# Optimization experiments

Hardware: AMD Instinct MI355X
Metric: run time of the kernel (lower is better)

The kernel has to match this reference:

```python
import jax, jax.numpy as jnp
import numpy as np

SINKHORN_ITERS = 50  # fixed iteration count (original uses err-tolerance while-loop)


def sinkhorn(M, a, b, lam):
    # M: [T, V] cost; a: [T, B] topic marginals; b: [V, B] word marginals
    K = jnp.exp(-M * lam)            # [T, V]
    u0 = jnp.ones_like(a) / a.shape[0]

    def step(u, _):
        v = b / (K.T @ u)            # [V, B]
        u = a / (K @ v)              # [T, B]
        return u, None

    u, _ = jax.lax.scan(step, u0, None, length=SINKHORN_ITERS)
    v = b / (K.T @ u)
    # per-document sinkhorn divergence: sum_t u_t * ((K*M) @ v)_t -> [B]
    return jnp.sum(u * ((K * M) @ v), axis=0)


def setup_inputs() -> dict:
    key = jax.random.key(0)
    kx, kt, kw, km, ke = jax.random.split(key, 5)
    B, T, V, E = 2048, 100, 20000, 256
    x = jax.random.uniform(kx, (B, V), dtype=jnp.float32)  # BoW-like weights
    doc_topic = jax.random.uniform(kt, (B, T), dtype=jnp.float32) + 1e-3
    doc_topic = doc_topic / jnp.sum(doc_topic, axis=1, keepdims=True)
    doc_word = jax.random.uniform(kw, (B, V), dtype=jnp.float32) + 1e-3
    doc_word = doc_word / jnp.sum(doc_word, axis=1, keepdims=True)
    M = jax.random.uniform(km, (T, V), dtype=jnp.float32)  # nonneg cost in [0,1)
    topic_embedding = jax.random.normal(ke, (T, E), dtype=jnp.float32)
    return {"x": x, "doc_topic": doc_topic, "doc_word": doc_word, "M": M,
            "topic_embedding": topic_embedding, "sh_alpha": 20,
            "rec_loss_weight": 100}


def reference(x, doc_topic, doc_word, M, topic_embedding, sh_alpha, rec_loss_weight):
    sh_loss = sinkhorn(M, doc_topic.T, doc_word.T, sh_alpha).mean()
    rec_log_probs = jax.nn.log_softmax(doc_topic @ (1.0 - M), axis=1)  # [B, V]
    rec_loss = -jnp.mean(jnp.sum(rec_log_probs * x, axis=1))
    joint_loss = rec_loss_weight * rec_loss + sh_loss
    return (rec_loss, sh_loss, joint_loss)
```

## Files before the change

### kernel.cpp

```cpp
#include <hip/hip_runtime.h>
#include <math.h>

#define B_   2048
#define T_   100
#define V_   20000
#define VP   20480
#define KP   128
#define TP   112
#define NC2  32
#define CH2  640
#define LDV  72
#define RXB  16

typedef short s8v __attribute__((ext_vector_type(8)));
typedef short s4v __attribute__((ext_vector_type(4)));
typedef float f4  __attribute__((ext_vector_type(4)));

__device__ __forceinline__ short f2bf(float f) {
    unsigned u = __builtin_bit_cast(unsigned, f);
    u += 0x7fffu + ((u >> 16) & 1u);
    return (short)(u >> 16);
}
__device__ __forceinline__ float bf2f(short h) {
    unsigned u = ((unsigned)(unsigned short)h) << 16;
    return __builtin_bit_cast(float, u);
}
#define MFMA(a,b,c) __builtin_amdgcn_mfma_f32_16x16x32_bf16((a),(b),(c),0,0,0)

__global__ void k_initKT(const float* __restrict__ M, const int* __restrict__ alpha,
                         short* __restrict__ A1, short* __restrict__ W1) {
    __shared__ float tile[32][33];
    float lam = (float)(*alpha);
    int v0 = blockIdx.x * 32, t0 = blockIdx.y * 32;
    int tx = threadIdx.x, ty = threadIdx.y;
    for (int j = 0; j < 4; ++j) {
        int t = t0 + ty + 8 * j, v = v0 + tx;
        tile[ty + 8 * j][tx] = (t < T_ && v < V_) ? M[(size_t)t * V_ + v] : 0.f;
    }
    __syncthreads();
    for (int j = 0; j < 4; ++j) {
        int t = t0 + tx, v = v0 + ty + 8 * j;
        float m = tile[tx][ty + 8 * j];
        bool valid = (t < T_) && (v < V_);
        A1[(size_t)v * KP + t] = valid ? f2bf(__expf(-m * lam)) : (short)0;
        W1[(size_t)v * KP + t] = valid ? f2bf(1.f - m) : (short)0;
    }
}

__global__ void k_initA2(const float* __restrict__ M, const int* __restrict__ alpha,
                         short* __restrict__ A2, short* __restrict__ A2M) {
    float lam = (float)(*alpha);
    size_t id = (size_t)blockIdx.x * 256 + threadIdx.x;
    int t = (int)(id / VP), v = (int)(id % VP);
    bool valid = (t < T_) && (v < V_);
    float m = valid ? M[(size_t)t * V_ + v] : 0.f;
    float k = valid ? __expf(-m * lam) : 0.f;
    A2[id]  = valid ? f2bf(k) : (short)0;
    A2M[id] = valid ? f2bf(k * m) : (short)0;
}

__global__ void k_init0(short* __restrict__ uTbf) {
    int id = blockIdx.x * 256 + threadIdx.x;
    int t = id & (KP - 1);
    uTbf[id] = (t < T_) ? f2bf(0.01f) : (short)0;
}

__global__ void k_castdw(const float* __restrict__ dw, short* __restrict__ dwbf) {
    size_t base = ((size_t)blockIdx.x * 256 + threadIdx.x) * 8;
    f4 x0 = __builtin_nontemporal_load((const f4*)(dw + base));
    f4 x1 = __builtin_nontemporal_load((const f4*)(dw + base + 4));
    s8v o;
    o[0]=f2bf(x0[0]); o[1]=f2bf(x0[1]); o[2]=f2bf(x0[2]); o[3]=f2bf(x0[3]);
    o[4]=f2bf(x1[0]); o[5]=f2bf(x1[1]); o[6]=f2bf(x1[2]); o[7]=f2bf(x1[3]);
    __builtin_nontemporal_store(o, (s8v*)(dwbf + base));
}

__global__ void k_castdt(const float* __restrict__ dt, short* __restrict__ dtbf) {
    int id = blockIdx.x * 256 + threadIdx.x;
    int b = id >> 7, t = id & (KP - 1);
    dtbf[id] = (t < T_) ? f2bf(dt[(size_t)b * T_ + t]) : (short)0;
}

__global__ __launch_bounds__(256, 2) void k_GF(const short* __restrict__ A1,
                                               const short* __restrict__ A2acc,
                                               const short* __restrict__ uT,
                                               const short* __restrict__ dwbf,
                                               float* __restrict__ part2) {
    __shared__ short vv[4][32 * LDV];
    int tid = threadIdx.x;
    int wave = tid >> 6, lane = tid & 63, q = lane >> 4, l16 = lane & 15;

    int l = blockIdx.x;
    int j = l & 31, bx = l >> 5;
    int c = ((j & 7) << 2) | (j >> 3);
    int v0 = c * CH2;
    int b0 = bx * 128 + wave * 32;
    short* buf = vv[wave];

    s8v au[2][4];
#pragma unroll
    for (int cb = 0; cb < 2; ++cb)
#pragma unroll
        for (int ks = 0; ks < 4; ++ks)
            au[cb][ks] = *(const s8v*)(uT + (size_t)(b0 + cb * 16 + l16) * KP + ks * 32 + q * 8);

    f4 acc2[7][2];
#pragma unroll
    for (int tt = 0; tt < 7; ++tt) { acc2[tt][0] = (f4)0.f; acc2[tt][1] = (f4)0.f; }

    for (int s = 0; s < 10; ++s) {
        int vs = v0 + s * 64;
        s4v dwv[2][4];
#pragma unroll
        for (int cb = 0; cb < 2; ++cb)
#pragma unroll
            for (int vt = 0; vt < 4; ++vt) {
                int vg = vs + vt * 16 + q * 4;
                dwv[cb][vt] = (vg < V_)
                    ? __builtin_nontemporal_load(
                          (const s4v*)(dwbf + (size_t)(b0 + cb * 16 + l16) * V_ + vg))
                    : (s4v)0;
            }
        s8v a2r[2][7];
#pragma unroll
        for (int ks2 = 0; ks2 < 2; ++ks2)
#pragma unroll
            for (int tt = 0; tt < 7; ++tt)
                a2r[ks2][tt] = *(const s8v*)(A2acc + (size_t)(tt * 16 + l16) * VP
                                             + vs + ks2 * 32 + q * 8);
        f4 acc1[2][4];
#pragma unroll
        for (int cb = 0; cb < 2; ++cb)
#pragma unroll
            for (int vt = 0; vt < 4; ++vt) acc1[cb][vt] = (f4)0.f;
#pragma unroll
        for (int ks = 0; ks < 4; ++ks) {
            int ko = ks * 32 + q * 8;
            s8v bv[4];
#pragma unroll
            for (int vt = 0; vt < 4; ++vt)
                bv[vt] = *(const s8v*)(A1 + (size_t)(vs + vt * 16 + l16) * KP + ko);
#pragma unroll
            for (int cb = 0; cb < 2; ++cb)
#pragma unroll
                for (int vt = 0; vt < 4; ++vt)
                    acc1[cb][vt] = MFMA(bv[vt], au[cb][ks], acc1[cb][vt]);
        }
#pragma unroll
        for (int cb = 0; cb < 2; ++cb)
#pragma unroll
            for (int vt = 0; vt < 4; ++vt) {
                int vg = vs + vt * 16 + q * 4;
                s4v o;
                if (vg < V_) {
#pragma unroll
                    for (int r = 0; r < 4; ++r)
                        o[r] = f2bf(bf2f(dwv[cb][vt][r]) * __builtin_amdgcn_rcpf(acc1[cb][vt][r]));
                } else {
                    o = (s4v)0;
                }
                *(s4v*)(buf + (cb * 16 + l16) * LDV + vt * 16 + q * 4) = o;
            }
#pragma unroll
        for (int ks2 = 0; ks2 < 2; ++ks2) {
            int ko = ks2 * 32 + q * 8;
            s8v bb[2];
#pragma unroll
            for (int cb = 0; cb < 2; ++cb)
                bb[cb] = *(const s8v*)(buf + (cb * 16 + l16) * LDV + ko);
#pragma unroll
            for (int tt = 0; tt < 7; ++tt)
#pragma unroll
                for (int cb = 0; cb < 2; ++cb)
                    acc2[tt][cb] = MFMA(a2r[ks2][tt], bb[cb], acc2[tt][cb]);
        }
        __builtin_amdgcn_s_barrier();
    }
#pragma unroll
    for (int tt = 0; tt < 7; ++tt)
#pragma unroll
        for (int cb = 0; cb < 2; ++cb) {
            int bg = b0 + cb * 16 + l16;
            __builtin_nontemporal_store(acc2[tt][cb],
                (f4*)(part2 + ((size_t)c * B_ + bg) * TP + tt * 16 + q * 4));
        }
}

__global__ void k_R(const float* __restrict__ part2, const float* __restrict__ dt,
                    float* __restrict__ uf, short* __restrict__ uTbf,
                    float* __restrict__ kmvf, int mode) {
    int id = blockIdx.x * 256 + threadIdx.x;
    int b = id / 28, t4 = (id % 28) * 4;
    f4 s = (f4)0.f;
    for (int c = 0; c < NC2; ++c)
        s += __builtin_nontemporal_load(
                 (const f4*)(part2 + ((size_t)c * B_ + b) * TP + t4));
    if (mode == 0) {
#pragma unroll
        for (int j = 0; j < 4; ++j) {
            int t = t4 + j;
            float v = (t < T_) ? dt[(size_t)b * T_ + t] / s[j] : 0.f;
            uf[(size_t)b * TP + t] = v;
            uTbf[(size_t)b * KP + t] = f2bf(v);
        }
    } else {
#pragma unroll
        for (int j = 0; j < 4; ++j) kmvf[(size_t)b * TP + t4 + j] = s[j];
    }
}

__global__ __launch_bounds__(256, 4) void k_rec(const short* __restrict__ dtbf,
                                                const short* __restrict__ W1,
                                                const float* __restrict__ x,
                                                float* __restrict__ recP) {
    int tid = threadIdx.x;
    int wave = tid >> 6, lane = tid & 63, q = lane >> 4, l16 = lane & 15;
    int xb = blockIdx.x;
    int v0 = xb * (RXB == 16 ? 1280 : 0);
    int b0 = blockIdx.y * 64;
    int bg = b0 + wave * 16 + l16;
    s8v a[4];
#pragma unroll
    for (int ks = 0; ks < 4; ++ks)
        a[ks] = *(const s8v*)(dtbf + (size_t)bg * KP + ks * 32 + q * 8);
    float se = 0.f, sxl = 0.f, sx = 0.f;
    for (int st = 0; st < 5; ++st) {
        int vs = v0 + st * 256;
        f4 acc[16];
#pragma unroll
        for (int vt = 0; vt < 16; ++vt) acc[vt] = (f4)0.f;
#pragma unroll
        for (int ks = 0; ks < 4; ++ks) {
            int ko = ks * 32 + q * 8;
#pragma unroll
            for (int vt = 0; vt < 16; ++vt) {
                s8v w = *(const s8v*)(W1 + (size_t)(vs + vt * 16 + l16) * KP + ko);
                acc[vt] = MFMA(w, a[ks], acc[vt]);
            }
        }
#pragma unroll
        for (int vt = 0; vt < 16; ++vt) {
            int vg = vs + vt * 16 + q * 4;
            if (vg < V_) {
                f4 xv = __builtin_nontemporal_load(
                            (const f4*)(x + (size_t)bg * V_ + vg));
#pragma unroll
                for (int r = 0; r < 4; ++r) {
                    float lo = acc[vt][r];
                    se += __expf(lo); sxl += lo * xv[r]; sx += xv[r];
                }
            }
        }
    }
    se  += __shfl_xor(se, 16, 64);  se  += __shfl_xor(se, 32, 64);
    sxl += __shfl_xor(sxl, 16, 64); sxl += __shfl_xor(sxl, 32, 64);
    sx  += __shfl_xor(sx, 16, 64);  sx  += __shfl_xor(sx, 32, 64);
    if (q == 0) {
        recP[((size_t)xb * 3 + 0) * B_ + bg] = se;
        recP[((size_t)xb * 3 + 1) * B_ + bg] = sxl;
        recP[((size_t)xb * 3 + 2) * B_ + bg] = sx;
    }
}

__global__ void k_div(const float* __restrict__ uf, const float* __restrict__ kmvf,
                      const float* __restrict__ recP, float* __restrict__ divb,
                      float* __restrict__ recSE, float* __restrict__ recSXL,
                      float* __restrict__ recSX) {
    int b = blockIdx.x * 256 + threadIdx.x;
    if (b >= B_) return;
    float s = 0.f;
    for (int t = 0; t < TP; ++t) s += uf[(size_t)b * TP + t] * kmvf[(size_t)b * TP + t];
    divb[b] = s;
    float se = 0.f, sxl = 0.f, sx = 0.f;
    for (int xb = 0; xb < RXB; ++xb) {
        se  += recP[((size_t)xb * 3 + 0) * B_ + b];
        sxl += recP[((size_t)xb * 3 + 1) * B_ + b];
        sx  += recP[((size_t)xb * 3 + 2) * B_ + b];
    }
    recSE[b] = se; recSXL[b] = sxl; recSX[b] = sx;
}

__global__ void k_final(const float* __restrict__ divb, const float* __restrict__ recSE,
                        const float* __restrict__ recSXL, const float* __restrict__ recSX,
                        const int* __restrict__ wptr, float* __restrict__ out) {
    __shared__ float sA[256], sB[256];
    int tid = threadIdx.x;
    float accS = 0.f, accR = 0.f;
    for (int b = tid; b < B_; b += 256) {
        accS += divb[b];
        accR += recSXL[b] - logf(recSE[b]) * recSX[b];
    }
    sA[tid] = accS; sB[tid] = accR;
    __syncthreads();
    for (int s = 128; s > 0; s >>= 1) {
        if (tid < s) { sA[tid] += sA[tid + s]; sB[tid] += sB[tid + s]; }
        __syncthreads();
    }
    if (tid == 0) {
        float sh = sA[0] / (float)B_;
        float rec = -sB[0] / (float)B_;
        out[0] = rec;
        out[1] = sh;
        out[2] = (float)(*wptr) * rec + sh;
    }
}

extern "C" void kernel_launch(void* const* d_in, const int* in_sizes, int n_in,
                              void* d_out, int out_size, void* d_ws, size_t ws_size,
                              hipStream_t stream) {
    const float* x  = (const float*)d_in[0];
    const float* dt = (const float*)d_in[1];
    const float* dw = (const float*)d_in[2];
    const float* M  = (const float*)d_in[3];
    const int* alpha = (const int*)d_in[5];
    const int* wrec  = (const int*)d_in[6];
    float* out = (float*)d_out;

    char* p = (char*)d_ws;
    short* A1   = (short*)p; p += (size_t)VP * KP * 2;
    short* W1   = (short*)p; p += (size_t)VP * KP * 2;
    short* A2   = (short*)p; p += (size_t)TP * VP * 2;
    short* A2M  = (short*)p; p += (size_t)TP * VP * 2;
    short* uTbf = (short*)p; p += (size_t)B_ * KP * 2;
    short* dtbf = (short*)p; p += (size_t)B_ * KP * 2;
    short* dwbf = (short*)p; p += (size_t)B_ * V_ * 2;
    float* part2 = (float*)p; p += (size_t)NC2 * B_ * TP * 4;
    float* uf    = (float*)p; p += (size_t)B_ * TP * 4;
    float* kmvf  = (float*)p; p += (size_t)B_ * TP * 4;
    float* recP  = (float*)p; p += (size_t)RXB * 3 * B_ * 4;
    float* recSE  = (float*)p; p += B_ * 4;
    float* recSXL = (float*)p; p += B_ * 4;
    float* recSX  = (float*)p; p += B_ * 4;
    float* divb   = (float*)p; p += B_ * 4;

    k_initKT<<<dim3(VP / 32, 4), dim3(32, 8), 0, stream>>>(M, alpha, A1, W1);
    k_initA2<<<(TP * VP) / 256, 256, 0, stream>>>(M, alpha, A2, A2M);
    k_init0<<<(B_ * KP) / 256, 256, 0, stream>>>(uTbf);
    k_castdw<<<(B_ * V_) / (256 * 8), 256, 0, stream>>>(dw, dwbf);
    k_castdt<<<(B_ * KP) / 256, 256, 0, stream>>>(dt, dtbf);
    k_rec<<<dim3(RXB, B_ / 64), 256, 0, stream>>>(dtbf, W1, x, recP);

    for (int it = 0; it < 50; ++it) {
        k_GF<<<dim3((B_ / 128) * NC2), 256, 0, stream>>>(A1, A2, uTbf, dwbf, part2);
        k_R<<<(B_ * 28) / 256, 256, 0, stream>>>(part2, dt, uf, uTbf, kmvf, 0);
    }
    k_GF<<<dim3((B_ / 128) * NC2), 256, 0, stream>>>(A1, A2M, uTbf, dwbf, part2);
    k_R<<<(B_ * 28) / 256, 256, 0, stream>>>(part2, dt, uf, uTbf, kmvf, 1);
    k_div<<<B_ / 256, 256, 0, stream>>>(uf, kmvf, recP, divb, recSE, recSXL, recSX);
    k_final<<<1, 256, 0, stream>>>(divb, recSE, recSXL, recSX, wrec, out);
}
```

Before: 5.677 ms.

## Halve GF chunk size, raise occupancy, and restructure rec kernel tiling

k_GF now splits V into 64 chunks of 320 instead of 32 of 640, with a matching blockIdx swizzle, and declares three blocks per CU instead of two. A2acc operands are loaded inside the MFMA loop instead of being preloaded into registers, and the per-iteration barrier is removed, all to cut register pressure and raise occupancy. k_rec is retiled to 128-column blocks (158 along V), with x loads issued up front to overlap the MFMA work, and nontemporal load hints are dropped. The cost is more partial sums for k_R to reduce and more A2acc loads on the critical path.

```diff
diff --git a/kernel.cpp b/kernel.cpp
--- a/kernel.cpp
+++ b/kernel.cpp
@@ -7,10 +7,10 @@
 #define VP   20480
 #define KP   128
 #define TP   112
-#define NC2  32
-#define CH2  640
+#define NC2  64
+#define CH2  320
 #define LDV  72
-#define RXB  16
+#define RXB  158
 
 typedef short s8v __attribute__((ext_vector_type(8)));
 typedef short s4v __attribute__((ext_vector_type(4)));
@@ -81,7 +81,7 @@
     dtbf[id] = (t < T_) ? f2bf(dt[(size_t)b * T_ + t]) : (short)0;
 }
 
-__global__ __launch_bounds__(256, 2) void k_GF(const short* __restrict__ A1,
+__global__ __launch_bounds__(256, 3) void k_GF(const short* __restrict__ A1,
                                                const short* __restrict__ A2acc,
                                                const short* __restrict__ uT,
                                                const short* __restrict__ dwbf,
@@ -91,8 +91,8 @@
     int wave = tid >> 6, lane = tid & 63, q = lane >> 4, l16 = lane & 15;
 
     int l = blockIdx.x;
-    int j = l & 31, bx = l >> 5;
-    int c = ((j & 7) << 2) | (j >> 3);
+    int j = l & 63, bx = l >> 6;
+    int c = ((j & 7) << 3) | (j >> 3);
     int v0 = c * CH2;
     int b0 = bx * 128 + wave * 32;
     short* buf = vv[wave];
@@ -108,7 +108,7 @@
 #pragma unroll
     for (int tt = 0; tt < 7; ++tt) { acc2[tt][0] = (f4)0.f; acc2[tt][1] = (f4)0.f; }
 
-    for (int s = 0; s < 10; ++s) {
+    for (int s = 0; s < 5; ++s) {
         int vs = v0 + s * 64;
         s4v dwv[2][4];
 #pragma unroll
@@ -117,17 +117,9 @@
             for (int vt = 0; vt < 4; ++vt) {
                 int vg = vs + vt * 16 + q * 4;
                 dwv[cb][vt] = (vg < V_)
-                    ? __builtin_nontemporal_load(
-                          (const s4v*)(dwbf + (size_t)(b0 + cb * 16 + l16) * V_ + vg))
+                    ? *(const s4v*)(dwbf + (size_t)(b0 + cb * 16 + l16) * V_ + vg)
                     : (s4v)0;
             }
-        s8v a2r[2][7];
-#pragma unroll
-        for (int ks2 = 0; ks2 < 2; ++ks2)
-#pragma unroll
-            for (int tt = 0; tt < 7; ++tt)
-                a2r[ks2][tt] = *(const s8v*)(A2acc + (size_t)(tt * 16 + l16) * VP
-                                             + vs + ks2 * 32 + q * 8);
         f4 acc1[2][4];
 #pragma unroll
         for (int cb = 0; cb < 2; ++cb)
@@ -169,12 +161,13 @@
             for (int cb = 0; cb < 2; ++cb)
                 bb[cb] = *(const s8v*)(buf + (cb * 16 + l16) * LDV + ko);
 #pragma unroll
-            for (int tt = 0; tt < 7; ++tt)
+            for (int tt = 0; tt < 7; ++tt) {
+                s8v a = *(const s8v*)(A2acc + (size_t)(tt * 16 + l16) * VP + vs + ko);
 #pragma unroll
                 for (int cb = 0; cb < 2; ++cb)
-                    acc2[tt][cb] = MFMA(a2r[ks2][tt], bb[cb], acc2[tt][cb]);
-        }
-        __builtin_amdgcn_s_barrier();
+                    acc2[tt][cb] = MFMA(a, bb[cb], acc2[tt][cb]);
+            }
+        }
     }
 #pragma unroll
     for (int tt = 0; tt < 7; ++tt)
@@ -216,39 +209,40 @@
     int tid = threadIdx.x;
     int wave = tid >> 6, lane = tid & 63, q = lane >> 4, l16 = lane & 15;
     int xb = blockIdx.x;
-    int v0 = xb * (RXB == 16 ? 1280 : 0);
+    int v0 = xb * 128;
     int b0 = blockIdx.y * 64;
     int bg = b0 + wave * 16 + l16;
+    f4 xv[8];
+#pragma unroll
+    for (int vt = 0; vt < 8; ++vt) {
+        int vg = v0 + vt * 16 + q * 4;
+        xv[vt] = (vg < V_) ? *(const f4*)(x + (size_t)bg * V_ + vg) : (f4)0.f;
+    }
     s8v a[4];
 #pragma unroll
     for (int ks = 0; ks < 4; ++ks)
         a[ks] = *(const s8v*)(dtbf + (size_t)bg * KP + ks * 32 + q * 8);
+    f4 acc[8];
+#pragma unroll
+    for (int vt = 0; vt < 8; ++vt) acc[vt] = (f4)0.f;
+#pragma unroll
+    for (int ks = 0; ks < 4; ++ks) {
+        int ko = ks * 32 + q * 8;
+#pragma unroll
+        for (int vt = 0; vt < 8; ++vt) {
+            s8v w = *(const s8v*)(W1 + (size_t)(v0 + vt * 16 + l16) * KP + ko);
+            acc[vt] = MFMA(w, a[ks], acc[vt]);
+        }
+    }
     float se = 0.f, sxl = 0.f, sx = 0.f;
-    for (int st = 0; st < 5; ++st) {
-        int vs = v0 + st * 256;
-        f4 acc[16];
-#pragma unroll
-        for (int vt = 0; vt < 16; ++vt) acc[vt] = (f4)0.f;
-#pragma unroll
-        for (int ks = 0; ks < 4; ++ks) {
-            int ko = ks * 32 + q * 8;
-#pragma unroll
-            for (int vt = 0; vt < 16; ++vt) {
-                s8v w = *(const s8v*)(W1 + (size_t)(vs + vt * 16 + l16) * KP + ko);
-                acc[vt] = MFMA(w, a[ks], acc[vt]);
-            }
-        }
-#pragma unroll
-        for (int vt = 0; vt < 16; ++vt) {
-            int vg = vs + vt * 16 + q * 4;
-            if (vg < V_) {
-                f4 xv = __builtin_nontemporal_load(
-                            (const f4*)(x + (size_t)bg * V_ + vg));
-#pragma unroll
-                for (int r = 0; r < 4; ++r) {
-                    float lo = acc[vt][r];
-                    se += __expf(lo); sxl += lo * xv[r]; sx += xv[r];
-                }
+#pragma unroll
+    for (int vt = 0; vt < 8; ++vt) {
+        int vg = v0 + vt * 16 + q * 4;
+        if (vg < V_) {
+#pragma unroll
+            for (int r = 0; r < 4; ++r) {
+                float lo = acc[vt][r];
+                se += __expf(lo); sxl += lo * xv[vt][r]; sx += xv[vt][r];
             }
         }
     }
```

Measured after the change: 6.790 ms. 19.6% more time.
